# Kernel optimization log

Hardware: AMD Instinct MI355X
Metric: run time of the kernel (lower is better)

The kernel has to match this reference:

```python
import jax, jax.numpy as jnp
import numpy as np

N_HEAD = 16

def setup_inputs() -> dict:
    key = jax.random.key(0)
    ks = jax.random.split(key, 5)
    B, T, D = 2, 2048, 1024
    k = D // N_HEAD
    scale = 0.02
    return {
        'x': jax.random.normal(ks[0], (B, T, D), dtype=jnp.float32),
        'Wq': jax.random.normal(ks[1], (D, D), dtype=jnp.float32) * scale,
        'Wk': jax.random.normal(ks[2], (D, k), dtype=jnp.float32) * scale,
        'Wv': jax.random.normal(ks[3], (D, k), dtype=jnp.float32) * scale,
        'Wo': jax.random.normal(ks[4], (D, D), dtype=jnp.float32) * scale,
    }

def reference(x, Wq, Wk, Wv, Wo):
    B, T, D = x.shape
    h = N_HEAD
    k = D // h
    Q = (x @ Wq).reshape(B, T, h, k)          # per-head queries
    K = x @ Wk                                 # single shared K head: (B,T,k)
    V = x @ Wv                                 # single shared V head: (B,T,k)
    scores = jnp.einsum('bthk,bsk->bhts', Q, K) / jnp.sqrt(jnp.float32(k))
    causal = jnp.tril(jnp.ones((T, T), dtype=bool))  # (T,T)
    scores = jnp.where(causal[None, None, :, :], scores, -jnp.inf)
    A = jax.nn.softmax(scores, axis=-1)        # (B,h,T,T)
    Y = jnp.einsum('bhts,bsk->bthk', A, V).reshape(B, T, D)
    return Y @ Wo
```

## Files before the change

### kernel.cpp

```cpp
#include <hip/hip_runtime.h>
#include <hip/hip_bf16.h>
#include <stdint.h>

typedef short short8 __attribute__((ext_vector_type(8)));
typedef float f32x4 __attribute__((ext_vector_type(4)));

constexpr int SEQ   = 2048;
constexpr int DM    = 1024;
constexpr int NHEAD = 16;
constexpr int HD    = 64;
constexpr int LDQ   = 1152;
constexpr int BATCH = 2;

__device__ __forceinline__ unsigned short f2bf(float f) {
    union { float f; uint32_t u; } v; v.f = f;
    uint32_t u = v.u;
    uint32_t r = (u + 0x7fffu + ((u >> 16) & 1u)) >> 16;
    return (unsigned short)r;
}

typedef __attribute__((address_space(1))) const void gvoid_t;
typedef __attribute__((address_space(3))) void lvoid_t;
__device__ __forceinline__ void gload16(const void* g, void* l) {
    __builtin_amdgcn_global_load_lds((gvoid_t*)g, (lvoid_t*)l, 16, 0, 0);
}

__global__ __launch_bounds__(256) void cast_x_kernel(
        const float* __restrict__ x, unsigned short* __restrict__ xb, int n) {
    int i = (blockIdx.x * 256 + threadIdx.x) * 4;
    if (i >= n) return;
    const float4 v = *(const float4*)(x + i);
    ushort4 o;
    o.x = f2bf(v.x); o.y = f2bf(v.y); o.z = f2bf(v.z); o.w = f2bf(v.w);
    *(ushort4*)(xb + i) = o;
}

__global__ __launch_bounds__(256) void prep_w_kernel(
        const float* __restrict__ Wq, const float* __restrict__ Wk,
        const float* __restrict__ Wv, const float* __restrict__ Wo,
        unsigned short* __restrict__ wtq, unsigned short* __restrict__ wot) {
    __shared__ unsigned short tile[32][33];
    int z = blockIdx.z;
    const float* W; unsigned short* Wt; int C;
    if (z == 0)      { W = Wq; Wt = wtq;                              C = DM; }
    else if (z == 1) { W = Wk; Wt = wtq + (size_t)DM * DM;            C = HD; }
    else if (z == 2) { W = Wv; Wt = wtq + (size_t)(DM + HD) * DM;     C = HD; }
    else             { W = Wo; Wt = wot;                              C = DM; }
    int c0 = blockIdx.x * 32, r0 = blockIdx.y * 32;
    if (c0 >= C) return;
    int tx = threadIdx.x & 31, ty = threadIdx.x >> 5;
    for (int i = ty; i < 32; i += 8)
        tile[i][tx] = f2bf(W[(size_t)(r0 + i) * C + (c0 + tx)]);
    __syncthreads();
    for (int i = ty; i < 32; i += 8)
        Wt[(size_t)(c0 + i) * DM + (r0 + tx)] = tile[tx][i];
}

__global__ __launch_bounds__(256) void transpose_v_kernel(
        const unsigned short* __restrict__ QKV, unsigned short* __restrict__ Vt) {
    __shared__ unsigned short tile[32][33];
    int b = blockIdx.z;
    int s0 = blockIdx.x * 32;
    int d0 = blockIdx.y * 32;
    int tx = threadIdx.x & 31, ty = threadIdx.x >> 5;
    const unsigned short* src = QKV + (size_t)b * SEQ * LDQ + DM + HD;
    for (int i = ty; i < 32; i += 8)
        tile[i][tx] = src[(size_t)(s0 + i) * LDQ + d0 + tx];
    __syncthreads();
    unsigned short* dst = Vt + (size_t)b * HD * SEQ;
    for (int i = ty; i < 32; i += 8)
        dst[(size_t)(d0 + i) * SEQ + s0 + tx] = tile[tx][i];
}

__global__ __launch_bounds__(256) void gemm_bt_kernel(
        const unsigned short* __restrict__ A,
        const unsigned short* __restrict__ Bt,
        void* __restrict__ Cout,
        int M, int N, int K, int out_bf16) {
    __shared__ unsigned short ldsA[2][128 * 32];
    __shared__ unsigned short ldsB[2][64 * 32];
    int lane = threadIdx.x & 63, wave = threadIdx.x >> 6;
    int ln = lane & 15, quad = lane >> 4;
    int wm = wave >> 1, wn = wave & 1;
    int m0 = blockIdx.y * 128, n0 = blockIdx.x * 64;

    int srow = lane >> 2, scol = (lane & 3) * 8;
    const unsigned short* gA0 = A + (size_t)(m0 + wave * 32 + srow) * K + scol;
    const unsigned short* gA1 = gA0 + (size_t)16 * K;
    const unsigned short* gB0 = Bt + (size_t)(n0 + wave * 16 + srow) * K + scol;

    f32x4 acc[4][2];
    for (int i = 0; i < 4; ++i)
        for (int jj = 0; jj < 2; ++jj) acc[i][jj] = f32x4{0, 0, 0, 0};

    for (int k0 = 0; k0 < K; k0 += 64) {
#pragma unroll
        for (int hh = 0; hh < 2; ++hh) {
            gload16(gA0 + k0 + hh * 32, &ldsA[hh][wave * 1024]);
            gload16(gA1 + k0 + hh * 32, &ldsA[hh][wave * 1024 + 512]);
            gload16(gB0 + k0 + hh * 32, &ldsB[hh][wave * 512]);
        }
        __syncthreads();
        short8 aF[2][4], bF[2][2];
#pragma unroll
        for (int hh = 0; hh < 2; ++hh) {
#pragma unroll
            for (int i = 0; i < 4; ++i)
                aF[hh][i] = *(const short8*)&ldsA[hh][(wm * 64 + i * 16 + ln) * 32 + quad * 8];
#pragma unroll
            for (int jj = 0; jj < 2; ++jj)
                bF[hh][jj] = *(const short8*)&ldsB[hh][(wn * 32 + jj * 16 + ln) * 32 + quad * 8];
        }
#pragma unroll
        for (int hh = 0; hh < 2; ++hh)
#pragma unroll
            for (int mt = 0; mt < 4; ++mt)
#pragma unroll
                for (int nt = 0; nt < 2; ++nt)
                    acc[mt][nt] = __builtin_amdgcn_mfma_f32_16x16x32_bf16(
                        aF[hh][mt], bF[hh][nt], acc[mt][nt], 0, 0, 0);
        __syncthreads();
    }

    if (out_bf16) {
        unsigned short* C = (unsigned short*)Cout;
#pragma unroll
        for (int mt = 0; mt < 4; ++mt)
            for (int nt = 0; nt < 2; ++nt)
                for (int r = 0; r < 4; ++r) {
                    int row = m0 + wm * 64 + mt * 16 + quad * 4 + r;
                    int col = n0 + wn * 32 + nt * 16 + ln;
                    C[(size_t)row * N + col] = f2bf(acc[mt][nt][r]);
                }
    } else {
        float* C = (float*)Cout;
#pragma unroll
        for (int mt = 0; mt < 4; ++mt)
            for (int nt = 0; nt < 2; ++nt)
                for (int r = 0; r < 4; ++r) {
                    int row = m0 + wm * 64 + mt * 16 + quad * 4 + r;
                    int col = n0 + wn * 32 + nt * 16 + ln;
                    C[(size_t)row * N + col] = acc[mt][nt][r];
                }
    }
}

__global__ __launch_bounds__(256) void attn_kernel(
        const unsigned short* __restrict__ QKV,
        const unsigned short* __restrict__ Vt,
        unsigned short* __restrict__ Y) {
    __shared__ unsigned short ldsK[2][32 * 64];
    __shared__ unsigned short ldsV[2][64 * 32];
    __shared__ unsigned short pbuf[4][16][40];

    int lane = threadIdx.x & 63, wave = threadIdx.x >> 6;
    int ln = lane & 15, quad = lane >> 4;
    int bid = blockIdx.x;
    int jg = 31 - (bid >> 5);
    int bh = bid & 31;
    int h = bh & 15, b = bh >> 4;
    int q0 = (jg * 4 + wave) * 16;
    const size_t baseRow = (size_t)b * SEQ;
    const unsigned short* Vb = Vt + (size_t)b * HD * SEQ;

    int tK_r = threadIdx.x >> 3;
    int tK_cb = (threadIdx.x & 7) ^ (tK_r & 7);
    const unsigned short* gK = QKV + (baseRow + tK_r) * LDQ + DM + tK_cb * 8;
    int tV_r = threadIdx.x >> 2;
    int tV_cb = (threadIdx.x & 3) ^ ((tV_r >> 1) & 3);
    const unsigned short* gV = Vb + (size_t)tV_r * SEQ + tV_cb * 8;

    short8 aQ0, aQ1;
    {
        const unsigned short* qp = QKV + (baseRow + q0 + ln) * LDQ + h * HD + quad * 8;
        aQ0 = *(const short8*)(qp);
        aQ1 = *(const short8*)(qp + 32);
    }

    float lsum[4] = {0.f, 0.f, 0.f, 0.f};
    f32x4 o[4];
    for (int nt = 0; nt < 4; ++nt) o[nt] = f32x4{0, 0, 0, 0};

    const float c_exp = 0.1803368802f;
    const int nsteps = 2 * jg + 2;
    const int mysmax = q0 + 15;

    gload16(gK, &ldsK[0][wave * 512]);
    gload16(gV, &ldsV[0][wave * 512]);

    for (int it = 0; it < nsteps; ++it) {
        int s0 = it * 32;
        __syncthreads();
        if (it + 1 < nsteps) {
            int sn = s0 + 32;
            gload16(gK + (size_t)sn * LDQ, &ldsK[(it + 1) & 1][wave * 512]);
            gload16(gV + sn,               &ldsV[(it + 1) & 1][wave * 512]);
        }
        if (s0 <= mysmax) {
            const unsigned short* Kb = ldsK[it & 1];
            const unsigned short* Vbuf = ldsV[it & 1];
            short8 bK[2][2];
#pragma unroll
            for (int c = 0; c < 2; ++c) {
                int r = c * 16 + ln;
                bK[c][0] = *(const short8*)&Kb[r * 64 + ((quad ^ (ln & 7)) * 8)];
                bK[c][1] = *(const short8*)&Kb[r * 64 + (((quad + 4) ^ (ln & 7)) * 8)];
            }
            short8 bV[4];
#pragma unroll
            for (int nt = 0; nt < 4; ++nt) {
                int row = nt * 16 + ln;
                bV[nt] = *(const short8*)&Vbuf[row * 32 + ((quad ^ ((ln >> 1) & 3)) * 8)];
            }

            float p[2][4];
#pragma unroll
            for (int c = 0; c < 2; ++c) {
                f32x4 s = {0, 0, 0, 0};
                s = __builtin_amdgcn_mfma_f32_16x16x32_bf16(aQ0, bK[c][0], s, 0, 0, 0);
                s = __builtin_amdgcn_mfma_f32_16x16x32_bf16(aQ1, bK[c][1], s, 0, 0, 0);
                int srow = s0 + c * 16 + ln;
                for (int r = 0; r < 4; ++r) {
                    int ti = q0 + quad * 4 + r;
                    float e = __builtin_exp2f(s[r] * c_exp);
                    p[c][r] = (srow > ti) ? 0.f : e;
                }
            }
#pragma unroll
            for (int r = 0; r < 4; ++r) lsum[r] += p[0][r] + p[1][r];

#pragma unroll
            for (int c = 0; c < 2; ++c)
                for (int r = 0; r < 4; ++r)
                    pbuf[wave][quad * 4 + r][c * 16 + ln] = f2bf(p[c][r]);
            short8 aP = *(const short8*)&pbuf[wave][ln][quad * 8];
#pragma unroll
            for (int nt = 0; nt < 4; ++nt)
                o[nt] = __builtin_amdgcn_mfma_f32_16x16x32_bf16(aP, bV[nt], o[nt], 0, 0, 0);
        }
    }

    for (int off = 1; off < 16; off <<= 1)
#pragma unroll
        for (int r = 0; r < 4; ++r) lsum[r] += __shfl_xor(lsum[r], off);
#pragma unroll
    for (int r = 0; r < 4; ++r) {
        float inv = 1.0f / lsum[r];
        int t_idx = q0 + quad * 4 + r;
        unsigned short* yp = Y + (baseRow + t_idx) * DM + h * HD + ln;
        for (int nt = 0; nt < 4; ++nt)
            yp[nt * 16] = f2bf(o[nt][r] * inv);
    }
}

extern "C" void kernel_launch(void* const* d_in, const int* in_sizes, int n_in,
                              void* d_out, int out_size, void* d_ws, size_t ws_size,
                              hipStream_t stream) {
    const float* x  = (const float*)d_in[0];
    const float* Wq = (const float*)d_in[1];
    const float* Wk = (const float*)d_in[2];
    const float* Wv = (const float*)d_in[3];
    const float* Wo = (const float*)d_in[4];
    float* out = (float*)d_out;

    char* ws = (char*)d_ws;
    unsigned short* xb  = (unsigned short*)(ws);
    unsigned short* Vt  = (unsigned short*)(ws);
    unsigned short* wtq = (unsigned short*)(ws + 8388608);
    unsigned short* wot = (unsigned short*)(ws + 10747904);
    unsigned short* qkv = (unsigned short*)(ws + 12845056);
    unsigned short* y   = (unsigned short*)(ws + 22282240);

    const int BT = BATCH * SEQ;

    hipLaunchKernelGGL(cast_x_kernel, dim3(BT * DM / 4 / 256), dim3(256), 0, stream,
                       x, xb, BT * DM);
    hipLaunchKernelGGL(prep_w_kernel, dim3(DM / 32, DM / 32, 4), dim3(256), 0, stream,
                       Wq, Wk, Wv, Wo, wtq, wot);

    hipLaunchKernelGGL(gemm_bt_kernel, dim3(LDQ / 64, BT / 128), dim3(256), 0, stream,
                       xb, wtq, (void*)qkv, BT, LDQ, DM, 1);

    hipLaunchKernelGGL(transpose_v_kernel, dim3(SEQ / 32, HD / 32, BATCH), dim3(256), 0, stream,
                       qkv, Vt);

    hipLaunchKernelGGL(attn_kernel, dim3(32 * 32), dim3(256), 0, stream,
                       qkv, Vt, y);

    hipLaunchKernelGGL(gemm_bt_kernel, dim3(DM / 64, BT / 128), dim3(256), 0, stream,
                       y, wot, (void*)out, BT, DM, DM, 0);
}
```

Measured before the change: 187.6 us.

## Double-buffer GEMM, widen attention KV tile to 64, fuse V transpose into QKV GEMM

The GEMM now double-buffers its LDS tiles, so the next K-slice is loaded while the current one is multiplied, and it drops the trailing barrier. The QKV GEMM epilogue writes V transposed directly, which removes the separate transpose kernel launch. The attention kernel processes 64 keys per step instead of 32, halving barrier and loop overhead. Only the final diagonal step applies masking, and P is converted by truncation instead of round-to-nearest. These changes double the LDS footprint, which may lower occupancy, and the truncating bf16 conversion adds slight bias to P.

Result: faster. 173.5 us (-7.5%).

```diff
diff --git a/kernel.cpp b/kernel.cpp
--- a/kernel.cpp
+++ b/kernel.cpp
@@ -56,29 +56,14 @@
         Wt[(size_t)(c0 + i) * DM + (r0 + tx)] = tile[tx][i];
 }
 
-__global__ __launch_bounds__(256) void transpose_v_kernel(
-        const unsigned short* __restrict__ QKV, unsigned short* __restrict__ Vt) {
-    __shared__ unsigned short tile[32][33];
-    int b = blockIdx.z;
-    int s0 = blockIdx.x * 32;
-    int d0 = blockIdx.y * 32;
-    int tx = threadIdx.x & 31, ty = threadIdx.x >> 5;
-    const unsigned short* src = QKV + (size_t)b * SEQ * LDQ + DM + HD;
-    for (int i = ty; i < 32; i += 8)
-        tile[i][tx] = src[(size_t)(s0 + i) * LDQ + d0 + tx];
-    __syncthreads();
-    unsigned short* dst = Vt + (size_t)b * HD * SEQ;
-    for (int i = ty; i < 32; i += 8)
-        dst[(size_t)(d0 + i) * SEQ + s0 + tx] = tile[tx][i];
-}
-
 __global__ __launch_bounds__(256) void gemm_bt_kernel(
         const unsigned short* __restrict__ A,
         const unsigned short* __restrict__ Bt,
         void* __restrict__ Cout,
+        unsigned short* __restrict__ VtOut,
         int M, int N, int K, int out_bf16) {
-    __shared__ unsigned short ldsA[2][128 * 32];
-    __shared__ unsigned short ldsB[2][64 * 32];
+    __shared__ unsigned short ldsA[2][2][128 * 32];
+    __shared__ unsigned short ldsB[2][2][64 * 32];
     int lane = threadIdx.x & 63, wave = threadIdx.x >> 6;
     int ln = lane & 15, quad = lane >> 4;
     int wm = wave >> 1, wn = wave & 1;
@@ -93,23 +78,30 @@
     for (int i = 0; i < 4; ++i)
         for (int jj = 0; jj < 2; ++jj) acc[i][jj] = f32x4{0, 0, 0, 0};
 
-    for (int k0 = 0; k0 < K; k0 += 64) {
+    auto stage = [&](int k0, int buf) {
 #pragma unroll
         for (int hh = 0; hh < 2; ++hh) {
-            gload16(gA0 + k0 + hh * 32, &ldsA[hh][wave * 1024]);
-            gload16(gA1 + k0 + hh * 32, &ldsA[hh][wave * 1024 + 512]);
-            gload16(gB0 + k0 + hh * 32, &ldsB[hh][wave * 512]);
-        }
+            gload16(gA0 + k0 + hh * 32, &ldsA[buf][hh][wave * 1024]);
+            gload16(gA1 + k0 + hh * 32, &ldsA[buf][hh][wave * 1024 + 512]);
+            gload16(gB0 + k0 + hh * 32, &ldsB[buf][hh][wave * 512]);
+        }
+    };
+
+    stage(0, 0);
+    int niter = K >> 6;
+    for (int it = 0; it < niter; ++it) {
         __syncthreads();
+        if (it + 1 < niter) stage((it + 1) << 6, (it + 1) & 1);
+        int buf = it & 1;
         short8 aF[2][4], bF[2][2];
 #pragma unroll
         for (int hh = 0; hh < 2; ++hh) {
 #pragma unroll
             for (int i = 0; i < 4; ++i)
-                aF[hh][i] = *(const short8*)&ldsA[hh][(wm * 64 + i * 16 + ln) * 32 + quad * 8];
+                aF[hh][i] = *(const short8*)&ldsA[buf][hh][(wm * 64 + i * 16 + ln) * 32 + quad * 8];
 #pragma unroll
             for (int jj = 0; jj < 2; ++jj)
-                bF[hh][jj] = *(const short8*)&ldsB[hh][(wn * 32 + jj * 16 + ln) * 32 + quad * 8];
+                bF[hh][jj] = *(const short8*)&ldsB[buf][hh][(wn * 32 + jj * 16 + ln) * 32 + quad * 8];
         }
 #pragma unroll
         for (int hh = 0; hh < 2; ++hh)
@@ -119,7 +111,6 @@
                 for (int nt = 0; nt < 2; ++nt)
                     acc[mt][nt] = __builtin_amdgcn_mfma_f32_16x16x32_bf16(
                         aF[hh][mt], bF[hh][nt], acc[mt][nt], 0, 0, 0);
-        __syncthreads();
     }
 
     if (out_bf16) {
@@ -132,6 +123,17 @@
                     int col = n0 + wn * 32 + nt * 16 + ln;
                     C[(size_t)row * N + col] = f2bf(acc[mt][nt][r]);
                 }
+        if (VtOut != nullptr && n0 == DM + HD) {
+#pragma unroll
+            for (int mt = 0; mt < 4; ++mt)
+                for (int nt = 0; nt < 2; ++nt)
+                    for (int r = 0; r < 4; ++r) {
+                        int row = m0 + wm * 64 + mt * 16 + quad * 4 + r;
+                        int d = wn * 32 + nt * 16 + ln;
+                        int bb = row >> 11, s = row & 2047;
+                        VtOut[((size_t)bb * HD + d) * SEQ + s] = f2bf(acc[mt][nt][r]);
+                    }
+        }
     } else {
         float* C = (float*)Cout;
 #pragma unroll
@@ -149,9 +151,9 @@
         const unsigned short* __restrict__ QKV,
         const unsigned short* __restrict__ Vt,
         unsigned short* __restrict__ Y) {
-    __shared__ unsigned short ldsK[2][32 * 64];
-    __shared__ unsigned short ldsV[2][64 * 32];
-    __shared__ unsigned short pbuf[4][16][40];
+    __shared__ unsigned short ldsK[2][64 * 64];
+    __shared__ unsigned short ldsV[2][64 * 64];
+    __shared__ unsigned short pbuf[4][16][72];
 
     int lane = threadIdx.x & 63, wave = threadIdx.x >> 6;
     int ln = lane & 15, quad = lane >> 4;
@@ -163,12 +165,20 @@
     const size_t baseRow = (size_t)b * SEQ;
     const unsigned short* Vb = Vt + (size_t)b * HD * SEQ;
 
-    int tK_r = threadIdx.x >> 3;
-    int tK_cb = (threadIdx.x & 7) ^ (tK_r & 7);
-    const unsigned short* gK = QKV + (baseRow + tK_r) * LDQ + DM + tK_cb * 8;
-    int tV_r = threadIdx.x >> 2;
-    int tV_cb = (threadIdx.x & 3) ^ ((tV_r >> 1) & 3);
-    const unsigned short* gV = Vb + (size_t)tV_r * SEQ + tV_cb * 8;
+    int t = threadIdx.x;
+    int trow = t >> 3, tcb = t & 7;
+    int cbg = tcb ^ (trow & 7);
+    const unsigned short* gK = QKV + (baseRow + trow) * LDQ + DM + cbg * 8;
+    const unsigned short* gV = Vb + (size_t)trow * SEQ + cbg * 8;
+    int dstoff = trow * 64 + tcb * 8;
+
+    auto stageKV = [&](int s0n, int buf) {
+#pragma unroll
+        for (int rr = 0; rr < 2; ++rr) {
+            gload16(gK + (size_t)(s0n + 32 * rr) * LDQ, &ldsK[buf][dstoff + rr * 2048]);
+            gload16(gV + (size_t)32 * rr * SEQ + s0n,   &ldsV[buf][dstoff + rr * 2048]);
+        }
+    };
 
     short8 aQ0, aQ1;
     {
@@ -182,63 +192,53 @@
     for (int nt = 0; nt < 4; ++nt) o[nt] = f32x4{0, 0, 0, 0};
 
     const float c_exp = 0.1803368802f;
-    const int nsteps = 2 * jg + 2;
-    const int mysmax = q0 + 15;
-
-    gload16(gK, &ldsK[0][wave * 512]);
-    gload16(gV, &ldsV[0][wave * 512]);
-
-    for (int it = 0; it < nsteps; ++it) {
-        int s0 = it * 32;
+
+    auto computeStep = [&](int s0, int buf, bool partial) {
+        const unsigned short* Kb = ldsK[buf];
+        const unsigned short* Vf = ldsV[buf];
+#pragma unroll
+        for (int c = 0; c < 4; ++c) {
+            int kbase = s0 + c * 16;
+            if (partial && kbase > q0 + 15) {
+#pragma unroll
+                for (int r = 0; r < 4; ++r)
+                    pbuf[wave][quad * 4 + r][c * 16 + ln] = 0;
+                continue;
+            }
+            short8 k0f = *(const short8*)&Kb[(c * 16 + ln) * 64 + ((quad ^ (ln & 7)) * 8)];
+            short8 k1f = *(const short8*)&Kb[(c * 16 + ln) * 64 + (((4 + quad) ^ (ln & 7)) * 8)];
+            f32x4 s = {0, 0, 0, 0};
+            s = __builtin_amdgcn_mfma_f32_16x16x32_bf16(aQ0, k0f, s, 0, 0, 0);
+            s = __builtin_amdgcn_mfma_f32_16x16x32_bf16(aQ1, k1f, s, 0, 0, 0);
+            bool diag = partial && (kbase + 15 > q0);
+#pragma unroll
+            for (int r = 0; r < 4; ++r) {
+                float e = __builtin_exp2f(s[r] * c_exp);
+                if (diag && (kbase + ln > q0 + quad * 4 + r)) e = 0.f;
+                lsum[r] += e;
+                pbuf[wave][quad * 4 + r][c * 16 + ln] =
+                    (unsigned short)(__float_as_uint(e) >> 16);
+            }
+        }
+        short8 aP0 = *(const short8*)&pbuf[wave][ln][quad * 8];
+        short8 aP1 = *(const short8*)&pbuf[wave][ln][32 + quad * 8];
+#pragma unroll
+        for (int nt = 0; nt < 4; ++nt) {
+            short8 v0 = *(const short8*)&Vf[(nt * 16 + ln) * 64 + ((quad ^ (ln & 7)) * 8)];
+            short8 v1 = *(const short8*)&Vf[(nt * 16 + ln) * 64 + (((4 + quad) ^ (ln & 7)) * 8)];
+            o[nt] = __builtin_amdgcn_mfma_f32_16x16x32_bf16(aP0, v0, o[nt], 0, 0, 0);
+            o[nt] = __builtin_amdgcn_mfma_f32_16x16x32_bf16(aP1, v1, o[nt], 0, 0, 0);
+        }
+    };
+
+    stageKV(0, 0);
+    for (int it = 0; it < jg; ++it) {
         __syncthreads();
-        if (it + 1 < nsteps) {
-            int sn = s0 + 32;
-            gload16(gK + (size_t)sn * LDQ, &ldsK[(it + 1) & 1][wave * 512]);
-            gload16(gV + sn,               &ldsV[(it + 1) & 1][wave * 512]);
-        }
-        if (s0 <= mysmax) {
-            const unsigned short* Kb = ldsK[it & 1];
-            const unsigned short* Vbuf = ldsV[it & 1];
-            short8 bK[2][2];
-#pragma unroll
-            for (int c = 0; c < 2; ++c) {
-                int r = c * 16 + ln;
-                bK[c][0] = *(const short8*)&Kb[r * 64 + ((quad ^ (ln & 7)) * 8)];
-                bK[c][1] = *(const short8*)&Kb[r * 64 + (((quad + 4) ^ (ln & 7)) * 8)];
-            }
-            short8 bV[4];
-#pragma unroll
-            for (int nt = 0; nt < 4; ++nt) {
-                int row = nt * 16 + ln;
-                bV[nt] = *(const short8*)&Vbuf[row * 32 + ((quad ^ ((ln >> 1) & 3)) * 8)];
-            }
-
-            float p[2][4];
-#pragma unroll
-            for (int c = 0; c < 2; ++c) {
-                f32x4 s = {0, 0, 0, 0};
-                s = __builtin_amdgcn_mfma_f32_16x16x32_bf16(aQ0, bK[c][0], s, 0, 0, 0);
-                s = __builtin_amdgcn_mfma_f32_16x16x32_bf16(aQ1, bK[c][1], s, 0, 0, 0);
-                int srow = s0 + c * 16 + ln;
-                for (int r = 0; r < 4; ++r) {
-                    int ti = q0 + quad * 4 + r;
-                    float e = __builtin_exp2f(s[r] * c_exp);
-                    p[c][r] = (srow > ti) ? 0.f : e;
-                }
-            }
-#pragma unroll
-            for (int r = 0; r < 4; ++r) lsum[r] += p[0][r] + p[1][r];
-
-#pragma unroll
-            for (int c = 0; c < 2; ++c)
-                for (int r = 0; r < 4; ++r)
-                    pbuf[wave][quad * 4 + r][c * 16 + ln] = f2bf(p[c][r]);
-            short8 aP = *(const short8*)&pbuf[wave][ln][quad * 8];
-#pragma unroll
-            for (int nt = 0; nt < 4; ++nt)
-                o[nt] = __builtin_amdgcn_mfma_f32_16x16x32_bf16(aP, bV[nt], o[nt], 0, 0, 0);
-        }
-    }
+        stageKV((it + 1) * 64, (it + 1) & 1);
+        computeStep(it * 64, it & 1, false);
+    }
+    __syncthreads();
+    computeStep(jg * 64, jg & 1, true);
 
     for (int off = 1; off < 16; off <<= 1)
 #pragma unroll
@@ -265,11 +265,11 @@
 
     char* ws = (char*)d_ws;
     unsigned short* xb  = (unsigned short*)(ws);
-    unsigned short* Vt  = (unsigned short*)(ws);
+    unsigned short* y   = (unsigned short*)(ws);
     unsigned short* wtq = (unsigned short*)(ws + 8388608);
     unsigned short* wot = (unsigned short*)(ws + 10747904);
     unsigned short* qkv = (unsigned short*)(ws + 12845056);
-    unsigned short* y   = (unsigned short*)(ws + 22282240);
+    unsigned short* Vt  = (unsigned short*)(ws + 22282240);
 
     const int BT = BATCH * SEQ;
 
@@ -279,14 +279,11 @@
                        Wq, Wk, Wv, Wo, wtq, wot);
 
     hipLaunchKernelGGL(gemm_bt_kernel, dim3(LDQ / 64, BT / 128), dim3(256), 0, stream,
-                       xb, wtq, (void*)qkv, BT, LDQ, DM, 1);
-
-    hipLaunchKernelGGL(transpose_v_kernel, dim3(SEQ / 32, HD / 32, BATCH), dim3(256), 0, stream,
-                       qkv, Vt);
+                       xb, wtq, (void*)qkv, Vt, BT, LDQ, DM, 1);
 
     hipLaunchKernelGGL(attn_kernel, dim3(32 * 32), dim3(256), 0, stream,
                        qkv, Vt, y);
 
     hipLaunchKernelGGL(gemm_bt_kernel, dim3(DM / 64, BT / 128), dim3(256), 0, stream,
-                       y, wot, (void*)out, BT, DM, DM, 0);
-}
+                       y, wot, (void*)out, nullptr, BT, DM, DM, 0);
+}
```
